# Optimization experiments

Measured on AMD Instinct MI355X. Metric: run time of the kernel, lower is better.

## Reference

```python
import jax, jax.numpy as jnp
import numpy as np

STRIDE = 16
NUM_A = 9
POS_TH, NEG_TH = 0.7, 0.3
FG, BG, IGN = 1.0, 0.0, 2.0
CAP = 128  # BATCH_SIZE * 0.5 for both fg and bg


def _generate_base_anchors(base_size=16, ratios=(0.5, 1.0, 2.0), scales=(8, 16, 32)):
    w = h = float(base_size)
    xc = yc = 0.5 * (base_size - 1)
    size = w * h
    out = []
    for r in ratios:
        ws = np.round(np.sqrt(size / r))
        hs = np.round(ws * r)
        for s in scales:
            W, H = ws * s, hs * s
            out.append([xc - 0.5 * (W - 1), yc - 0.5 * (H - 1),
                        xc + 0.5 * (W - 1), yc + 0.5 * (H - 1)])
    return np.asarray(out, dtype=np.float32)  # [9,4]


def _all_anchors(H, W):
    base = _generate_base_anchors()
    sx = np.arange(W, dtype=np.float32) * STRIDE
    sy = np.arange(H, dtype=np.float32) * STRIDE
    xs, ys = np.meshgrid(sx, sy)  # row-major over (h, w)
    shifts = np.stack([xs.ravel(), ys.ravel(), xs.ravel(), ys.ravel()], 1)
    return jnp.asarray((shifts[:, None, :] + base[None, :, :]).reshape(-1, 4))  # [H*W*9,4], order (h,w,a)


def _forward(scores, gt, im_w, im_h):
    H, W = scores.shape[2], scores.shape[3]
    anchors = _all_anchors(H, W)  # [N,4]
    valid = (anchors[:, 0] >= 0.) & (anchors[:, 1] >= 0.) & \
            (anchors[:, 2] < im_w) & (anchors[:, 3] < im_h)
    # pairwise IoU with +1 box convention
    aw = anchors[:, 2] - anchors[:, 0] + 1.
    ah = anchors[:, 3] - anchors[:, 1] + 1.
    a_area = jnp.where((aw > 0) & (ah > 0), aw * ah, 0.)
    gw = gt[:, 2] - gt[:, 0] + 1.
    gh = gt[:, 3] - gt[:, 1] + 1.
    g_area = jnp.where((gw > 0) & (gh > 0), gw * gh, 0.)
    ix1 = jnp.maximum(anchors[:, None, 0], gt[None, :, 0])
    iy1 = jnp.maximum(anchors[:, None, 1], gt[None, :, 1])
    ix2 = jnp.minimum(anchors[:, None, 2], gt[None, :, 2])
    iy2 = jnp.minimum(anchors[:, None, 3], gt[None, :, 3])
    iw = ix2 - ix1 + 1.
    ih = iy2 - iy1 + 1.
    inter = jnp.where((iw > 0) & (ih > 0), iw * ih, 0.)
    ovl = inter / (a_area[:, None] + g_area[None, :] - inter)  # [N,G]
    ovl_m = jnp.where(valid[:, None], ovl, -1.)  # exclude invalid anchors
    a_argmax = jnp.argmax(ovl, axis=1)           # best gt per anchor
    a_max = jnp.max(ovl, axis=1)
    g_max = jnp.max(ovl_m, axis=0)               # best (valid) anchor overlap per gt
    gt_fg = jnp.any(ovl_m == g_max[None, :], axis=1) & valid
    labels = jnp.where(valid & (a_max < NEG_TH), BG, IGN)
    labels = jnp.where(gt_fg, FG, labels)
    labels = jnp.where(valid & (a_max >= POS_TH), FG, labels)
    # random subsample fg/bg down to CAP each (matches npr.choice semantics in distribution)
    kf, kb = jax.random.split(jax.random.key(42))
    def subsample(lbl, mask, k):
        s = jnp.where(mask, jax.random.uniform(k, lbl.shape), jnp.inf)
        ranks = jnp.argsort(jnp.argsort(s))
        keep = ranks < jnp.minimum(jnp.sum(mask), CAP)
        return jnp.where(mask & ~keep, IGN, lbl)
    labels = subsample(labels, labels == FG, kf)
    labels = subsample(labels, labels == BG, kb)
    num_ni = jnp.sum(labels != IGN).astype(jnp.float32)
    gts = gt[a_argmax]
    ax = (anchors[:, 2] + anchors[:, 0]) * 0.5
    ay = (anchors[:, 3] + anchors[:, 1]) * 0.5
    gwm = gts[:, 2] - gts[:, 0] + 1.
    ghm = gts[:, 3] - gts[:, 1] + 1.
    gx = (gts[:, 2] + gts[:, 0]) * 0.5
    gy = (gts[:, 3] + gts[:, 1]) * 0.5
    adj = jnp.stack([(gx - ax) / aw, (gy - ay) / ah,
                     jnp.log(gwm / aw), jnp.log(ghm / ah)], axis=1)  # [N,4]
    adj = jnp.where(valid[:, None], adj, 0.)
    wts = jnp.where((labels == FG)[:, None], 1.0 / num_ni, 0.) * jnp.ones((1, 4), jnp.float32)
    labels_out = labels.reshape(1, H, W, NUM_A).transpose(0, 3, 1, 2) \
                       .reshape(1, 1, NUM_A * H, W).astype(jnp.int32)
    adj_out = adj.reshape(1, H, W, 4 * NUM_A).transpose(0, 3, 1, 2)
    wts_out = wts.reshape(1, H, W, 4 * NUM_A).transpose(0, 3, 1, 2)
    return labels_out, adj_out, wts_out


def setup_inputs() -> dict:
    key = jax.random.key(0)
    k1, k2, k3 = jax.random.split(key, 3)
    scores = jax.random.normal(k1, (1, 18, 256, 256), dtype=jnp.float32)
    G = 64
    cxy = jax.random.uniform(k2, (G, 2), minval=100., maxval=3900.)
    wh = jax.random.uniform(k3, (G, 2), minval=32., maxval=512.)
    x1y1 = jnp.clip(cxy - wh * 0.5, 0., 4095.)
    x2y2 = jnp.clip(cxy + wh * 0.5, 0., 4095.)
    gt = jnp.concatenate([x1y1, x2y2], axis=1)  # [G,4] = x1,y1,x2,y2
    return {"anchor_object_scores": scores, "ground_truth_boxes": gt,
            "im_w": 4096, "im_h": 4096}


def reference(anchor_object_scores, ground_truth_boxes, im_w, im_h):
    return _forward(anchor_object_scores, ground_truth_boxes, im_w, im_h)
```

## Files before the change

### kernel.cpp

```cpp
#include <hip/hip_runtime.h>
#include <stdint.h>


#define NUM_A 9
#define HW 65536
#define N_ANCH 589824
#define NG 64
#define CAPK 128u
#define NBIN 2048
#define BIN_SHIFT 12
#define CLIST_CAP 128u
#define NGRP 32
#define GATHER_CAP 2048u

#define LAB_BG 0u
#define LAB_FG 1u
#define LAB_IGN 2u

#define NBLK 576

#define OFF_HF    0
#define OFF_HB    NBIN
#define OFF_ROOTB (2*NBIN)
#define OFF_ROOTD (2*NBIN + 1)
#define OFF_SEL   4104
#define OFF_SUBB  4112
#define OFF_SUBD  (OFF_SUBB + 32*16)
#define OFF_CFLG  (OFF_SUBD + 32*16)
#define OFF_CCNTF (OFF_CFLG + 32*16)
#define OFF_CCNTB (OFF_CCNTF + 32*16)
#define CTRL_WORDS (OFF_CCNTB + 32*16)
#define OFF_CANDF CTRL_WORDS
#define OFF_CANDB (OFF_CANDF + 2*NGRP*CLIST_CAP)

#define MAGIC_C 0x5CA1AB1Eu

__constant__ float BA[NUM_A][4] = {
  { -84.f,  -40.f,  99.f,  55.f}, {-176.f,  -88.f, 191.f, 103.f},
  {-360.f, -184.f, 375.f, 199.f}, { -56.f,  -56.f,  71.f,  71.f},
  {-120.f, -120.f, 135.f, 135.f}, {-248.f, -248.f, 263.f, 263.f},
  { -36.f,  -80.f,  51.f,  95.f}, { -80.f, -168.f,  95.f, 183.f},
  {-168.f, -344.f, 183.f, 359.f}};

__host__ __device__ static inline void tf2x32(uint32_t k0, uint32_t k1,
                                              uint32_t x0, uint32_t x1,
                                              uint32_t* o0, uint32_t* o1) {
  const uint32_t ks2 = k0 ^ k1 ^ 0x1BD11BDAu;
#define TF_R(r) { x0 += x1; x1 = (x1 << (r)) | (x1 >> (32 - (r))); x1 ^= x0; }
  x0 += k0; x1 += k1;
  TF_R(13) TF_R(15) TF_R(26) TF_R(6)
  x0 += k1;  x1 += ks2 + 1u;
  TF_R(17) TF_R(29) TF_R(16) TF_R(24)
  x0 += ks2; x1 += k0 + 2u;
  TF_R(13) TF_R(15) TF_R(26) TF_R(6)
  x0 += k0;  x1 += k1 + 3u;
  TF_R(17) TF_R(29) TF_R(16) TF_R(24)
  x0 += k1;  x1 += ks2 + 4u;
  TF_R(13) TF_R(15) TF_R(26) TF_R(6)
  x0 += ks2; x1 += k0 + 5u;
#undef TF_R
  *o0 = x0; *o1 = x1;
}

__device__ static inline uint32_t mant_of(uint32_t k0, uint32_t k1, uint32_t n) {
  uint32_t o0, o1;
  tf2x32(k0, k1, 0u, n, &o0, &o1);
  return (o0 ^ o1) >> 9;
}

__device__ static inline float axis_best(float blo, float bhi, float glo,
                                         float ghi, int lo, int hi) {
  #pragma clang fp contract(off)
  float t1 = (ghi - bhi) * 0.0625f;
  float t2 = (glo - blo) * 0.0625f;
  float tmin = fminf(t1, t2), tmax = fmaxf(t1, t2);
  int c1 = (int)floorf(tmin), c2 = (int)ceilf(tmax);
  int cand0 = lo, cand1 = hi;
  int cand2 = min(max(c1,     lo), hi);
  int cand3 = min(max(c1 + 1, lo), hi);
  int cand4 = min(max(c2 - 1, lo), hi);
  int cand5 = min(max(c2,     lo), hi);
  float best = -3.0e38f;
  int cands[6] = {cand0, cand1, cand2, cand3, cand4, cand5};
  #pragma unroll
  for (int i = 0; i < 6; i++) {
    float s = (float)(cands[i] << 4);
    float v = fminf(bhi + s, ghi) - fmaxf(blo + s, glo) + 1.0f;
    best = fmaxf(best, v);
  }
  return best;
}

#define AG_LOAD(p)      __hip_atomic_load((p), __ATOMIC_RELAXED, __HIP_MEMORY_SCOPE_AGENT)
#define AG_STORE(p, v)  __hip_atomic_store((p), (v), __ATOMIC_RELAXED, __HIP_MEMORY_SCOPE_AGENT)

__global__ __launch_bounds__(256) void k_one(const float* __restrict__ gt,
                                             const int* __restrict__ imw_p,
                                             const int* __restrict__ imh_p,
                                             float* __restrict__ out_lab,
                                             float* __restrict__ out_adj,
                                             float* __restrict__ out_wts,
                                             uint32_t* __restrict__ ws,
                                             uint32_t kf0, uint32_t kf1,
                                             uint32_t kb0, uint32_t kb1) {
  #pragma clang fp contract(off)
  __shared__ uint64_t scB[GATHER_CAP];
  uint32_t* sh = (uint32_t*)scB;
  __shared__ float sg0[NG], sg1[NG], sg2[NG], sg3[NG], sga[NG], sgm[NG];
  __shared__ uint32_t sgmU[NG];
  __shared__ unsigned long long sMask[4];
  __shared__ int sAnyZero, sLastB, sLastD;
  __shared__ uint32_t sSel[8];
  __shared__ uint32_t sCnt[NGRP], sBase[NGRP], sTot;
  int tid = threadIdx.x;
  int b = blockIdx.x;
  int a = b >> 6, hb = (b & 63) << 2;

  {
    uint4* sh4 = (uint4*)sh;
    #pragma unroll
    for (int k = 0; k < 4; k++) sh4[tid + k * 256] = make_uint4(0, 0, 0, 0);
  }
  if (tid == 0) sAnyZero = 0;
  if (tid < NG) {
    const float4 g4 = ((const float4*)gt)[tid];
    sg0[tid] = g4.x; sg1[tid] = g4.y; sg2[tid] = g4.z; sg3[tid] = g4.w;
    float gw = g4.z - g4.x + 1.0f, gh = g4.w - g4.y + 1.0f;
    sga[tid] = (gw > 0.0f && gh > 0.0f) ? gw * gh : 0.0f;
    sgmU[tid] = 0u;
  }
  __syncthreads();

  {
    int imwi = imw_p[0], imhi = imh_p[0];
    for (int p = tid; p < NG * NUM_A; p += 256) {
      int g = p / NUM_A, q = p - g * NUM_A;
      float b0 = BA[q][0], b1 = BA[q][1], b2 = BA[q][2], b3 = BA[q][3];
      int ib0 = (int)b0, ib1 = (int)b1, ib2 = (int)b2, ib3 = (int)b3;
      int wlo = max(0, (-ib0 + 15) >> 4);
      int whi = min(255, (imwi - ib2 - 1) >> 4);
      int hlo = max(0, (-ib1 + 15) >> 4);
      int hhi = min(255, (imhi - ib3 - 1) >> 4);
      if (wlo > whi || hlo > hhi) continue;
      float iwb = axis_best(b0, b2, sg0[g], sg2[g], wlo, whi);
      float ihb = axis_best(b1, b3, sg1[g], sg3[g], hlo, hhi);
      float aw = b2 - b0 + 1.0f, ah = b3 - b1 + 1.0f;
      float aarea = aw * ah;
      float inter = (iwb > 0.0f && ihb > 0.0f) ? iwb * ihb : 0.0f;
      float den = aarea + sga[g] - inter;
      float o = inter / den;
      atomicMax(&sgmU[g], __float_as_uint(o));
    }
  }

  {
    int wv = tid >> 6, g = tid & 63;
    float sy = (float)((hb + wv) << 4);
    float ihp = fminf(BA[a][3] + sy, sg3[g]) - fmaxf(BA[a][1] + sy, sg1[g]) + 1.0f;
    unsigned long long mk = __ballot(ihp > 0.0f);
    if (g == 0) sMask[wv] = mk;
  }
  __syncthreads();
  if (tid < NG) {
    uint32_t mm = sgmU[tid];
    sgm[tid] = __uint_as_float(mm);
    if (mm == 0u) atomicOr(&sAnyZero, 1);
  }
  __syncthreads();

  float BA0 = BA[a][0], BA1 = BA[a][1], BA2 = BA[a][2], BA3 = BA[a][3];
  float imw = (float)imw_p[0], imh = (float)imh_p[0];
  int w = tid;
  float sx = (float)(w << 4);
  float A0 = BA0 + sx, A2 = BA2 + sx;
  float aw = A2 - A0 + 1.0f;
  float A1v[4], A3v[4];
  #pragma unroll
  for (int r = 0; r < 4; r++) {
    float sy = (float)((hb + r) << 4);
    A1v[r] = BA1 + sy; A3v[r] = BA3 + sy;
  }
  float ah = A3v[0] - A1v[0] + 1.0f;
  float aarea = aw * ah;
  bool xv = (A0 >= 0.0f) && (A2 < imw);

  unsigned long long mk0 = sMask[0], mk1 = sMask[1],
                     mk2 = sMask[2], mk3 = sMask[3];
  unsigned long long uni = mk0 | mk1 | mk2 | mk3;
  float amaxv[4] = {0.f, 0.f, 0.f, 0.f};
  int bgv[4] = {0, 0, 0, 0};
  uint32_t afv = 0u;
  while (uni) {
    int g = __ffsll(uni) - 1;
    uni &= uni - 1;
    float iw = fminf(A2, sg2[g]) - fmaxf(A0, sg0[g]) + 1.0f;
    if (!__any(iw > 0.0f)) continue;
    if (iw > 0.0f) {
      float base = aarea + sga[g];
      float gy1 = sg1[g], gy2 = sg3[g], gm = sgm[g];
#define DO_ROW(r, mk)                                                     \
      if ((mk >> g) & 1ull) {                                             \
        float ih = fminf(A3v[r], gy2) - fmaxf(A1v[r], gy1) + 1.0f;        \
        float inter = iw * ih;                                            \
        float o = inter / (base - inter);                                 \
        if (o > amaxv[r]) { amaxv[r] = o; bgv[r] = g; }                   \
        if (o == gm) afv |= (1u << r);                                    \
      }
      DO_ROW(0, mk0) DO_ROW(1, mk1) DO_ROW(2, mk2) DO_ROW(3, mk3)
#undef DO_ROW
    }
  }

  bool anyZ = (sAnyZero != 0);
  uint32_t lm[4];
  #pragma unroll
  for (int r = 0; r < 4; r++) {
    int hw = (hb + r) * 256 + w;
    bool valid = xv && (A1v[r] >= 0.0f) && (A3v[r] < imh);
    float amax = amaxv[r];
    bool anyfg = (((afv >> r) & 1u) || anyZ) && valid;
    uint32_t lab;
    if (!valid)                       lab = LAB_IGN;
    else if (anyfg || amax >= 0.7f)   lab = LAB_FG;
    else if (amax < 0.3f)             lab = LAB_BG;
    else                              lab = LAB_IGN;

    float adj0 = 0.f, adj1 = 0.f, adj2 = 0.f, adj3 = 0.f;
    if (valid) {
      int bg = bgv[r];
      float G0 = sg0[bg], G1 = sg1[bg], G2 = sg2[bg], G3 = sg3[bg];
      float ax = (A2 + A0) * 0.5f, ay = (A3v[r] + A1v[r]) * 0.5f;
      float gwm = G2 - G0 + 1.0f, ghm = G3 - G1 + 1.0f;
      float gx = (G2 + G0) * 0.5f, gy = (G3 + G1) * 0.5f;
      adj0 = (gx - ax) / aw;
      adj1 = (gy - ay) / ah;
      adj2 = logf(gwm / aw);
      adj3 = logf(ghm / ah);
    }
    int c4 = a * 4;
    out_adj[(c4 + 0) * HW + hw] = adj0;
    out_adj[(c4 + 1) * HW + hw] = adj1;
    out_adj[(c4 + 2) * HW + hw] = adj2;
    out_adj[(c4 + 3) * HW + hw] = adj3;

    uint32_t m = 0u;
    uint32_t n = (uint32_t)(hw * 9 + a);
    if (lab != LAB_IGN) {
      uint32_t kk0 = (lab == LAB_FG) ? kf0 : kb0;
      uint32_t kk1 = (lab == LAB_FG) ? kf1 : kb1;
      m = mant_of(kk0, kk1, n);
      atomicAdd(&sh[((lab == LAB_FG) ? 0 : NBIN) + (m >> BIN_SHIFT)], 1u);
    }
    lm[r] = (lab << 24) | m;
  }
  __syncthreads();

  for (int i = tid; i < 2 * NBIN; i += 256) {
    uint32_t v = sh[i];
    if (v) atomicAdd(&ws[OFF_HF + i], v);
  }
  asm volatile("s_waitcnt vmcnt(0)" ::: "memory");
  __syncthreads();

  if (tid == 0) {
    int last = 0;
    uint32_t v = atomicAdd(&ws[OFF_SUBB + (b & 31) * 16], 1u);
    if (v == 17u) {
      uint32_t r = atomicAdd(&ws[OFF_ROOTB], 1u);
      if (r == 31u) last = 1;
    }
    sLastB = last;
  }
  __syncthreads();
  if (sLastB) {
    for (int cls = 0; cls < 2; cls++) {
      uint32_t* hist = ws + (cls ? OFF_HB : OFF_HF);
      uint32_t* sel = ws + OFF_SEL + cls * 4;
      uint32_t loc[8], s = 0;
      #pragma unroll
      for (int j = 0; j < 8; j++) {
        loc[j] = AG_LOAD(&hist[tid * 8 + j]);
        s += loc[j];
      }
      sh[tid] = s; __syncthreads();
      for (int off = 1; off < 256; off <<= 1) {
        uint32_t v = (tid >= off) ? sh[tid - off] : 0u;
        __syncthreads();
        sh[tid] += v;
        __syncthreads();
      }
      uint32_t total = sh[255];
      uint32_t K = total < CAPK ? total : CAPK;
      if (tid == 0) {
        AG_STORE(&sel[3], K);
        if (K == 0u) {
          AG_STORE(&sel[0], 0xFFFFFFFFu); AG_STORE(&sel[1], 0u);
          AG_STORE(&sel[2], 0u);
        }
      }
      if (K > 0u) {
        uint32_t myC = sh[tid], pvC = (tid == 0) ? 0u : sh[tid - 1];
        if (myC >= K && pvC < K) {
          uint32_t cum = pvC; int bb = tid * 8;
          #pragma unroll
          for (int j = 0; j < 8; j++) {
            if (cum + loc[j] >= K) { bb = tid * 8 + j; break; }
            cum += loc[j];
          }
          AG_STORE(&sel[0], (uint32_t)bb); AG_STORE(&sel[1], cum);
          AG_STORE(&sel[2], K - cum);
        }
      }
      __syncthreads();
    }
    asm volatile("s_waitcnt vmcnt(0)" ::: "memory");
    __syncthreads();
    if (tid < 32) AG_STORE(&ws[OFF_CFLG + tid * 16], MAGIC_C);
  }

  if (tid == 0) {
    while (AG_LOAD(&ws[OFF_CFLG + (b & 31) * 16]) != MAGIC_C)
      __builtin_amdgcn_s_sleep(2);
  }
  __syncthreads();
  if (tid < 8) sSel[tid] = AG_LOAD(&ws[OFF_SEL + tid]);
  __syncthreads();
  uint32_t bf = sSel[0], Kf = sSel[3], bbn = sSel[4], Kb = sSel[7];
  float inv = 1.0f / (float)(Kf + Kb);

  uint32_t pushedMask = 0u;
  #pragma unroll
  for (int r = 0; r < 4; r++) {
    uint32_t lab = lm[r] >> 24;
    if (lab == LAB_IGN) continue;
    uint32_t m = lm[r] & 0x7FFFFFu;
    uint32_t bn = m >> BIN_SHIFT;
    uint32_t bnd = (lab == LAB_FG) ? bf : bbn;
    if (bn == bnd) {
      int hw = (hb + r) * 256 + w;
      uint32_t n = (uint32_t)(hw * 9 + a);
      uint32_t grp = (uint32_t)(b & 31);
      uint32_t cbase = (lab == LAB_FG) ? OFF_CCNTF : OFF_CCNTB;
      uint32_t idx = atomicAdd(&ws[cbase + grp * 16], 1u);
      if (idx < CLIST_CAP) {
        uint64_t* lst = (uint64_t*)(ws + ((lab == LAB_FG) ? OFF_CANDF
                                                          : OFF_CANDB)) +
                        grp * CLIST_CAP;
        AG_STORE(&lst[idx], ((uint64_t)m << 20) | (uint64_t)n);
        pushedMask |= (1u << r);
      }
    }
  }
  asm volatile("s_waitcnt vmcnt(0)" ::: "memory");
  __syncthreads();

  if (tid == 0) {
    int last = 0;
    uint32_t v = atomicAdd(&ws[OFF_SUBD + (b & 31) * 16], 1u);
    if (v == 17u) {
      uint32_t r = atomicAdd(&ws[OFF_ROOTD], 1u);
      if (r == 31u) last = 1;
    }
    sLastD = last;
  }
  __syncthreads();
  if (sLastD) {
    uint64_t* sc = scB;
    for (int cls = 0; cls < 2; cls++) {
      const uint64_t* lst0 =
          (const uint64_t*)(ws + (cls ? OFF_CANDB : OFF_CANDF));
      if (tid < NGRP) {
        uint32_t cg = AG_LOAD(&ws[(cls ? OFF_CCNTB : OFF_CCNTF) + tid * 16]);
        sCnt[tid] = cg < CLIST_CAP ? cg : CLIST_CAP;
      }
      __syncthreads();
      if (tid == 0) {
        uint32_t acc = 0;
        for (int g2 = 0; g2 < NGRP; g2++) { sBase[g2] = acc; acc += sCnt[g2]; }
        sTot = acc < GATHER_CAP ? acc : GATHER_CAP;
      }
      __syncthreads();
      for (uint32_t idx = tid; idx < NGRP * CLIST_CAP; idx += 256) {
        uint32_t grp = idx >> 7;
        uint32_t i = idx & (CLIST_CAP - 1u);
        if (i < sCnt[grp]) {
          uint32_t dst = sBase[grp] + i;
          if (dst < GATHER_CAP)
            sc[dst] = AG_LOAD(&lst0[grp * CLIST_CAP + i]);
        }
      }
      __syncthreads();
      uint32_t C = sTot;
      uint32_t need = AG_LOAD(&ws[OFF_SEL + cls * 4 + 2]);
      for (uint32_t i = tid; i < C; i += 256) {
        uint64_t k = sc[i];
        uint32_t rr = 0;
        for (uint32_t j = 0; j < C; j++) rr += (sc[j] < k) ? 1u : 0u;
        bool kept = (rr < need);
        uint32_t nn = (uint32_t)(k & 0xFFFFFu);
        uint32_t aa = nn % 9u, hww = nn / 9u;
        uint32_t tt = aa * HW + hww;
        float lv = kept ? (cls == 0 ? 1.0f : 0.0f) : 2.0f;
        float wvv = (kept && cls == 0) ? inv : 0.0f;
        AG_STORE(&out_lab[tt], lv);
        #pragma unroll
        for (int j2 = 0; j2 < 4; j2++)
          AG_STORE(&out_wts[(aa * 4 + j2) * HW + hww], wvv);
      }
      __syncthreads();
    }
  }

  #pragma unroll
  for (int r = 0; r < 4; r++) {
    if ((pushedMask >> r) & 1u) continue;
    int hw = (hb + r) * 256 + w;
    uint32_t lab = lm[r] >> 24;
    uint32_t m = lm[r] & 0x7FFFFFu;
    float outv = 2.0f, wv = 0.0f;
    if (lab == LAB_FG) {
      uint32_t bn = m >> BIN_SHIFT;
      if (bn < bf) { outv = 1.0f; wv = inv; }
    } else if (lab == LAB_BG) {
      uint32_t bn = m >> BIN_SHIFT;
      if (bn < bbn) outv = 0.0f;
    }
    out_lab[a * HW + hw] = outv;
    int c4 = a * 4;
    out_wts[(c4 + 0) * HW + hw] = wv;
    out_wts[(c4 + 1) * HW + hw] = wv;
    out_wts[(c4 + 2) * HW + hw] = wv;
    out_wts[(c4 + 3) * HW + hw] = wv;
  }
}

extern "C" void kernel_launch(void* const* d_in, const int* in_sizes, int n_in,
                              void* d_out, int out_size, void* d_ws,
                              size_t ws_size, hipStream_t stream) {
  const float* gt  = (const float*)d_in[1];
  const int*   imw = (const int*)d_in[2];
  const int*   imh = (const int*)d_in[3];
  float* out      = (float*)d_out;
  float* out_lab  = out;
  float* out_adj  = out + N_ANCH;
  float* out_wts  = out + 5 * N_ANCH;
  uint32_t* ws = (uint32_t*)d_ws;

  uint32_t kf0, kf1, kb0, kb1;
  tf2x32(0u, 42u, 0u, 0u, &kf0, &kf1);
  tf2x32(0u, 42u, 0u, 1u, &kb0, &kb1);

  hipMemsetAsync(ws, 0, CTRL_WORDS * sizeof(uint32_t), stream);
  hipLaunchKernelGGL(k_one, dim3(NBLK), dim3(256), 0, stream, gt, imw, imh,
                     out_lab, out_adj, out_wts, ws, kf0, kf1, kb0, kb1);
}
```

Baseline: 103.9 us.

## Replace histogram-based top-K selection with count-then-threshold sampling rounds

Drops the per-block shared-memory 2048-bin histograms and their global atomic merges for the fg and bg classes. Each block now only counts its fg and bg anchors. A single block derives a mantissa threshold aimed at about 512 candidates per class, and blocks push candidates below the threshold into hashed global lists. The last block of each round ranks those candidates to find the exact K-th key, or adjusts the threshold and triggers another round, up to 8 grid-wide rounds. This cuts atomic traffic, but each extra round adds another grid-wide spin barrier, and the result depends on every block being resident at once.

```diff
diff --git a/kernel.cpp b/kernel.cpp
--- a/kernel.cpp
+++ b/kernel.cpp
@@ -7,11 +7,6 @@
 #define N_ANCH 589824
 #define NG 64
 #define CAPK 128u
-#define NBIN 2048
-#define BIN_SHIFT 12
-#define CLIST_CAP 128u
-#define NGRP 32
-#define GATHER_CAP 2048u
 
 #define LAB_BG 0u
 #define LAB_FG 1u
@@ -19,19 +14,31 @@
 
 #define NBLK 576
 
-#define OFF_HF    0
-#define OFF_HB    NBIN
-#define OFF_ROOTB (2*NBIN)
-#define OFF_ROOTD (2*NBIN + 1)
-#define OFF_SEL   4104
-#define OFF_SUBB  4112
-#define OFF_SUBD  (OFF_SUBB + 32*16)
-#define OFF_CFLG  (OFF_SUBD + 32*16)
-#define OFF_CCNTF (OFF_CFLG + 32*16)
-#define OFF_CCNTB (OFF_CCNTF + 32*16)
-#define CTRL_WORDS (OFF_CCNTB + 32*16)
-#define OFF_CANDF CTRL_WORDS
-#define OFF_CANDB (OFF_CANDF + 2*NGRP*CLIST_CAP)
+#define NGRP 32
+#define GCAP 256u
+#define R_MAX 8
+#define TARGETC 512u
+#define TFULL (1u << 23)
+#define CLIMIT 1024u
+#define GATHER_CAP 2048u
+
+#define OFF_CNTF  0
+#define OFF_CNTB  512
+#define OFF_SUBB  1024
+#define OFF_ROOTB 1536
+#define OFF_SELB  1552
+#define OFF_CFLGB 1568
+#define OFF_RND   2080
+#define RSTRIDE   2080
+#define R_SUBD    0
+#define R_ROOTD   512
+#define R_DCMD    528
+#define R_CFLGD   544
+#define R_PCNTF   1056
+#define R_PCNTB   1568
+#define CTRL_WORDS (OFF_RND + R_MAX * RSTRIDE)
+#define OFF_LISTF CTRL_WORDS
+#define OFF_LISTB (OFF_LISTF + 2 * NGRP * GCAP)
 
 #define MAGIC_C 0x5CA1AB1Eu
 
@@ -105,23 +112,18 @@
                                              uint32_t kb0, uint32_t kb1) {
   #pragma clang fp contract(off)
   __shared__ uint64_t scB[GATHER_CAP];
-  uint32_t* sh = (uint32_t*)scB;
   __shared__ float sg0[NG], sg1[NG], sg2[NG], sg3[NG], sga[NG], sgm[NG];
   __shared__ uint32_t sgmU[NG];
   __shared__ unsigned long long sMask[4];
-  __shared__ int sAnyZero, sLastB, sLastD;
-  __shared__ uint32_t sSel[8];
-  __shared__ uint32_t sCnt[NGRP], sBase[NGRP], sTot;
+  __shared__ int sAnyZero, sLastB, sLastD, sOv;
+  __shared__ uint32_t sSel[12];
+  __shared__ uint32_t sCnt[NGRP], sBase[NGRP], sTot, sBkLo, sBkHi;
+  __shared__ uint32_t sCF, sCB;
   int tid = threadIdx.x;
   int b = blockIdx.x;
   int a = b >> 6, hb = (b & 63) << 2;
 
-  {
-    uint4* sh4 = (uint4*)sh;
-    #pragma unroll
-    for (int k = 0; k < 4; k++) sh4[tid + k * 256] = make_uint4(0, 0, 0, 0);
-  }
-  if (tid == 0) sAnyZero = 0;
+  if (tid == 0) { sAnyZero = 0; sCF = 0u; sCB = 0u; }
   if (tid < NG) {
     const float4 g4 = ((const float4*)gt)[tid];
     sg0[tid] = g4.x; sg1[tid] = g4.y; sg2[tid] = g4.z; sg3[tid] = g4.w;
@@ -213,6 +215,7 @@
 
   bool anyZ = (sAnyZero != 0);
   uint32_t lm[4];
+  uint32_t cfLoc = 0, cbLoc = 0;
   #pragma unroll
   for (int r = 0; r < 4; r++) {
     int hw = (hb + r) * 256 + w;
@@ -249,181 +252,209 @@
       uint32_t kk0 = (lab == LAB_FG) ? kf0 : kb0;
       uint32_t kk1 = (lab == LAB_FG) ? kf1 : kb1;
       m = mant_of(kk0, kk1, n);
-      atomicAdd(&sh[((lab == LAB_FG) ? 0 : NBIN) + (m >> BIN_SHIFT)], 1u);
+      if (lab == LAB_FG) cfLoc++; else cbLoc++;
     }
     lm[r] = (lab << 24) | m;
   }
-  __syncthreads();
-
-  for (int i = tid; i < 2 * NBIN; i += 256) {
-    uint32_t v = sh[i];
-    if (v) atomicAdd(&ws[OFF_HF + i], v);
-  }
-  asm volatile("s_waitcnt vmcnt(0)" ::: "memory");
+  if (cfLoc) atomicAdd(&sCF, cfLoc);
+  if (cbLoc) atomicAdd(&sCB, cbLoc);
   __syncthreads();
 
   if (tid == 0) {
+    if (sCF) atomicAdd(&ws[OFF_CNTF + (b & 31) * 16], sCF);
+    if (sCB) atomicAdd(&ws[OFF_CNTB + (b & 31) * 16], sCB);
+    asm volatile("s_waitcnt vmcnt(0)" ::: "memory");
     int last = 0;
     uint32_t v = atomicAdd(&ws[OFF_SUBB + (b & 31) * 16], 1u);
     if (v == 17u) {
-      uint32_t r = atomicAdd(&ws[OFF_ROOTB], 1u);
-      if (r == 31u) last = 1;
+      uint32_t q = atomicAdd(&ws[OFF_ROOTB], 1u);
+      if (q == 31u) last = 1;
     }
     sLastB = last;
   }
   __syncthreads();
   if (sLastB) {
-    for (int cls = 0; cls < 2; cls++) {
-      uint32_t* hist = ws + (cls ? OFF_HB : OFF_HF);
-      uint32_t* sel = ws + OFF_SEL + cls * 4;
-      uint32_t loc[8], s = 0;
-      #pragma unroll
-      for (int j = 0; j < 8; j++) {
-        loc[j] = AG_LOAD(&hist[tid * 8 + j]);
-        s += loc[j];
-      }
-      sh[tid] = s; __syncthreads();
-      for (int off = 1; off < 256; off <<= 1) {
-        uint32_t v = (tid >= off) ? sh[tid - off] : 0u;
+    if (tid < 32)       sCnt[tid] = AG_LOAD(&ws[OFF_CNTF + tid * 16]);
+    else if (tid < 64)  sBase[tid - 32] = AG_LOAD(&ws[OFF_CNTB + (tid - 32) * 16]);
+    __syncthreads();
+    if (tid == 0) {
+      uint32_t tf = 0, tb = 0;
+      for (int i = 0; i < 32; i++) { tf += sCnt[i]; tb += sBase[i]; }
+      uint32_t Kf_ = tf < CAPK ? tf : CAPK;
+      uint32_t Kb_ = tb < CAPK ? tb : CAPK;
+      uint32_t Tf_ = (tf <= TARGETC) ? TFULL
+                   : (uint32_t)(((unsigned long long)TARGETC << 23) / tf);
+      uint32_t Tb_ = (tb <= TARGETC) ? TFULL
+                   : (uint32_t)(((unsigned long long)TARGETC << 23) / tb);
+      if (Tf_ == 0u) Tf_ = 1u;
+      if (Tb_ == 0u) Tb_ = 1u;
+      AG_STORE(&ws[OFF_SELB + 0], Tf_); AG_STORE(&ws[OFF_SELB + 1], Tb_);
+      AG_STORE(&ws[OFF_SELB + 2], Kf_); AG_STORE(&ws[OFF_SELB + 3], Kb_);
+      AG_STORE(&ws[OFF_SELB + 4], tf);  AG_STORE(&ws[OFF_SELB + 5], tb);
+    }
+    asm volatile("s_waitcnt vmcnt(0)" ::: "memory");
+    __syncthreads();
+    if (tid < 32) AG_STORE(&ws[OFF_CFLGB + tid * 16], MAGIC_C);
+  }
+
+  if (tid == 0) {
+    while (AG_LOAD(&ws[OFF_CFLGB + (b & 31) * 16]) != MAGIC_C)
+      __builtin_amdgcn_s_sleep(2);
+  }
+  __syncthreads();
+  if (tid < 6) sSel[tid] = AG_LOAD(&ws[OFF_SELB + tid]);
+  __syncthreads();
+  uint32_t Tc[2] = {sSel[0], sSel[1]};
+  uint32_t Kf = sSel[2], Kb = sSel[3], totF = sSel[4], totB = sSel[5];
+  float inv = 1.0f / (float)(Kf + Kb);
+
+  uint32_t modeF = 0u, modeB = 0u;
+  uint64_t bkF = 0ull, bkB = 0ull;
+  bool doneSel = false;
+  for (int rnd = 0; rnd < R_MAX && !doneSel; rnd++) {
+    uint32_t base = OFF_RND + (uint32_t)rnd * RSTRIDE;
+    #pragma unroll
+    for (int r = 0; r < 4; r++) {
+      uint32_t lab = lm[r] >> 24;
+      if (lab == LAB_IGN) continue;
+      uint32_t m = lm[r] & 0x7FFFFFu;
+      int cls = (lab == LAB_FG) ? 0 : 1;
+      if (m < Tc[cls]) {
+        int hw = (hb + r) * 256 + w;
+        uint32_t n = (uint32_t)(hw * 9 + a);
+        uint32_t grp = (n * 2654435761u) >> 27;
+        uint32_t idx = atomicAdd(
+            &ws[base + (cls ? R_PCNTB : R_PCNTF) + grp * 16], 1u);
+        if (idx < GCAP) {
+          uint64_t* lst =
+              (uint64_t*)(ws + (cls ? OFF_LISTB : OFF_LISTF)) + grp * GCAP;
+          AG_STORE(&lst[idx], ((uint64_t)m << 20) | (uint64_t)n);
+        }
+      }
+    }
+    asm volatile("s_waitcnt vmcnt(0)" ::: "memory");
+    __syncthreads();
+    if (tid == 0) {
+      int last = 0;
+      uint32_t v = atomicAdd(&ws[base + R_SUBD + (b & 31) * 16], 1u);
+      if (v == 17u) {
+        uint32_t q = atomicAdd(&ws[base + R_ROOTD], 1u);
+        if (q == 31u) last = 1;
+      }
+      sLastD = last;
+    }
+    __syncthreads();
+    if (sLastD) {
+      uint32_t modes[2]; uint64_t bks[2]; int oks[2];
+      uint32_t Cs[2]; int ovs[2];
+      for (int cls = 0; cls < 2; cls++) {
+        uint32_t Kc = cls ? Kb : Kf;
+        uint32_t totc = cls ? totB : totF;
+        if (tid < 32)
+          sCnt[tid] = AG_LOAD(&ws[base + (cls ? R_PCNTB : R_PCNTF) + tid * 16]);
         __syncthreads();
-        sh[tid] += v;
+        if (tid == 0) {
+          uint32_t acc = 0; int ov = 0;
+          for (int g2 = 0; g2 < NGRP; g2++) {
+            uint32_t c2 = sCnt[g2];
+            if (c2 > GCAP) { ov = 1; c2 = GCAP; }
+            sBase[g2] = acc; acc += c2;
+          }
+          sTot = acc; sOv = ov;
+        }
         __syncthreads();
-      }
-      uint32_t total = sh[255];
-      uint32_t K = total < CAPK ? total : CAPK;
+        uint32_t C = sTot; int ov = sOv;
+        uint32_t mode = 0u; uint64_t bk = 0ull; int ok = 1;
+        if (Kc == 0u) { ok = 1; mode = 0u; }
+        else if (totc <= CAPK) { ok = (!ov && C == totc); mode = 1u; }
+        else {
+          ok = (!ov && C >= Kc && C <= CLIMIT &&
+                (totc > TARGETC || C == totc));
+          mode = 2u;
+        }
+        if (ok && mode == 2u) {
+          const uint64_t* lst0 =
+              (const uint64_t*)(ws + (cls ? OFF_LISTB : OFF_LISTF));
+          for (uint32_t idx = tid; idx < NGRP * GCAP; idx += 256) {
+            uint32_t g2 = idx >> 8, i = idx & 255u;
+            if (i < sCnt[g2]) {
+              uint32_t dst = sBase[g2] + i;
+              if (dst < GATHER_CAP)
+                scB[dst] = AG_LOAD(&lst0[g2 * GCAP + i]);
+            }
+          }
+          __syncthreads();
+          for (uint32_t i = tid; i < C; i += 256) {
+            uint64_t k = scB[i];
+            uint32_t rr = 0;
+            for (uint32_t j = 0; j < C; j++) rr += (scB[j] < k) ? 1u : 0u;
+            if (rr == Kc - 1u) {
+              sBkLo = (uint32_t)k; sBkHi = (uint32_t)(k >> 32);
+            }
+          }
+          __syncthreads();
+          bk = ((uint64_t)sBkHi << 32) | (uint64_t)sBkLo;
+        }
+        modes[cls] = mode; bks[cls] = bk; oks[cls] = ok;
+        Cs[cls] = C; ovs[cls] = ov;
+        __syncthreads();
+      }
+      uint32_t st = (oks[0] && oks[1]) ? 1u : 2u;
+      uint32_t TN[2];
+      for (int cls = 0; cls < 2; cls++) {
+        uint32_t t = Tc[cls];
+        if (!oks[cls]) {
+          if (ovs[cls] || Cs[cls] > CLIMIT) t = (t > 1u) ? (t >> 1) : 1u;
+          else { t = (t >= (TFULL >> 2)) ? TFULL : (t << 2); }
+        }
+        TN[cls] = t;
+      }
       if (tid == 0) {
-        AG_STORE(&sel[3], K);
-        if (K == 0u) {
-          AG_STORE(&sel[0], 0xFFFFFFFFu); AG_STORE(&sel[1], 0u);
-          AG_STORE(&sel[2], 0u);
-        }
-      }
-      if (K > 0u) {
-        uint32_t myC = sh[tid], pvC = (tid == 0) ? 0u : sh[tid - 1];
-        if (myC >= K && pvC < K) {
-          uint32_t cum = pvC; int bb = tid * 8;
-          #pragma unroll
-          for (int j = 0; j < 8; j++) {
-            if (cum + loc[j] >= K) { bb = tid * 8 + j; break; }
-            cum += loc[j];
-          }
-          AG_STORE(&sel[0], (uint32_t)bb); AG_STORE(&sel[1], cum);
-          AG_STORE(&sel[2], K - cum);
-        }
-      }
+        AG_STORE(&ws[base + R_DCMD + 0], st);
+        AG_STORE(&ws[base + R_DCMD + 1], modes[0]);
+        AG_STORE(&ws[base + R_DCMD + 2], (uint32_t)bks[0]);
+        AG_STORE(&ws[base + R_DCMD + 3], (uint32_t)(bks[0] >> 32));
+        AG_STORE(&ws[base + R_DCMD + 4], modes[1]);
+        AG_STORE(&ws[base + R_DCMD + 5], (uint32_t)bks[1]);
+        AG_STORE(&ws[base + R_DCMD + 6], (uint32_t)(bks[1] >> 32));
+        AG_STORE(&ws[base + R_DCMD + 7], TN[0]);
+        AG_STORE(&ws[base + R_DCMD + 8], TN[1]);
+      }
+      asm volatile("s_waitcnt vmcnt(0)" ::: "memory");
       __syncthreads();
-    }
-    asm volatile("s_waitcnt vmcnt(0)" ::: "memory");
-    __syncthreads();
-    if (tid < 32) AG_STORE(&ws[OFF_CFLG + tid * 16], MAGIC_C);
-  }
-
-  if (tid == 0) {
-    while (AG_LOAD(&ws[OFF_CFLG + (b & 31) * 16]) != MAGIC_C)
-      __builtin_amdgcn_s_sleep(2);
-  }
-  __syncthreads();
-  if (tid < 8) sSel[tid] = AG_LOAD(&ws[OFF_SEL + tid]);
-  __syncthreads();
-  uint32_t bf = sSel[0], Kf = sSel[3], bbn = sSel[4], Kb = sSel[7];
-  float inv = 1.0f / (float)(Kf + Kb);
-
-  uint32_t pushedMask = 0u;
+      if (tid < 32) AG_STORE(&ws[base + R_CFLGD + tid * 16], MAGIC_C);
+    }
+    if (tid == 0) {
+      while (AG_LOAD(&ws[base + R_CFLGD + (b & 31) * 16]) != MAGIC_C)
+        __builtin_amdgcn_s_sleep(2);
+    }
+    __syncthreads();
+    if (tid < 9) sSel[tid] = AG_LOAD(&ws[base + R_DCMD + tid]);
+    __syncthreads();
+    if (sSel[0] == 1u) {
+      modeF = sSel[1]; bkF = ((uint64_t)sSel[3] << 32) | (uint64_t)sSel[2];
+      modeB = sSel[4]; bkB = ((uint64_t)sSel[6] << 32) | (uint64_t)sSel[5];
+      doneSel = true;
+    } else {
+      Tc[0] = sSel[7]; Tc[1] = sSel[8];
+    }
+    __syncthreads();
+  }
+
   #pragma unroll
   for (int r = 0; r < 4; r++) {
-    uint32_t lab = lm[r] >> 24;
-    if (lab == LAB_IGN) continue;
-    uint32_t m = lm[r] & 0x7FFFFFu;
-    uint32_t bn = m >> BIN_SHIFT;
-    uint32_t bnd = (lab == LAB_FG) ? bf : bbn;
-    if (bn == bnd) {
-      int hw = (hb + r) * 256 + w;
-      uint32_t n = (uint32_t)(hw * 9 + a);
-      uint32_t grp = (uint32_t)(b & 31);
-      uint32_t cbase = (lab == LAB_FG) ? OFF_CCNTF : OFF_CCNTB;
-      uint32_t idx = atomicAdd(&ws[cbase + grp * 16], 1u);
-      if (idx < CLIST_CAP) {
-        uint64_t* lst = (uint64_t*)(ws + ((lab == LAB_FG) ? OFF_CANDF
-                                                          : OFF_CANDB)) +
-                        grp * CLIST_CAP;
-        AG_STORE(&lst[idx], ((uint64_t)m << 20) | (uint64_t)n);
-        pushedMask |= (1u << r);
-      }
-    }
-  }
-  asm volatile("s_waitcnt vmcnt(0)" ::: "memory");
-  __syncthreads();
-
-  if (tid == 0) {
-    int last = 0;
-    uint32_t v = atomicAdd(&ws[OFF_SUBD + (b & 31) * 16], 1u);
-    if (v == 17u) {
-      uint32_t r = atomicAdd(&ws[OFF_ROOTD], 1u);
-      if (r == 31u) last = 1;
-    }
-    sLastD = last;
-  }
-  __syncthreads();
-  if (sLastD) {
-    uint64_t* sc = scB;
-    for (int cls = 0; cls < 2; cls++) {
-      const uint64_t* lst0 =
-          (const uint64_t*)(ws + (cls ? OFF_CANDB : OFF_CANDF));
-      if (tid < NGRP) {
-        uint32_t cg = AG_LOAD(&ws[(cls ? OFF_CCNTB : OFF_CCNTF) + tid * 16]);
-        sCnt[tid] = cg < CLIST_CAP ? cg : CLIST_CAP;
-      }
-      __syncthreads();
-      if (tid == 0) {
-        uint32_t acc = 0;
-        for (int g2 = 0; g2 < NGRP; g2++) { sBase[g2] = acc; acc += sCnt[g2]; }
-        sTot = acc < GATHER_CAP ? acc : GATHER_CAP;
-      }
-      __syncthreads();
-      for (uint32_t idx = tid; idx < NGRP * CLIST_CAP; idx += 256) {
-        uint32_t grp = idx >> 7;
-        uint32_t i = idx & (CLIST_CAP - 1u);
-        if (i < sCnt[grp]) {
-          uint32_t dst = sBase[grp] + i;
-          if (dst < GATHER_CAP)
-            sc[dst] = AG_LOAD(&lst0[grp * CLIST_CAP + i]);
-        }
-      }
-      __syncthreads();
-      uint32_t C = sTot;
-      uint32_t need = AG_LOAD(&ws[OFF_SEL + cls * 4 + 2]);
-      for (uint32_t i = tid; i < C; i += 256) {
-        uint64_t k = sc[i];
-        uint32_t rr = 0;
-        for (uint32_t j = 0; j < C; j++) rr += (sc[j] < k) ? 1u : 0u;
-        bool kept = (rr < need);
-        uint32_t nn = (uint32_t)(k & 0xFFFFFu);
-        uint32_t aa = nn % 9u, hww = nn / 9u;
-        uint32_t tt = aa * HW + hww;
-        float lv = kept ? (cls == 0 ? 1.0f : 0.0f) : 2.0f;
-        float wvv = (kept && cls == 0) ? inv : 0.0f;
-        AG_STORE(&out_lab[tt], lv);
-        #pragma unroll
-        for (int j2 = 0; j2 < 4; j2++)
-          AG_STORE(&out_wts[(aa * 4 + j2) * HW + hww], wvv);
-      }
-      __syncthreads();
-    }
-  }
-
-  #pragma unroll
-  for (int r = 0; r < 4; r++) {
-    if ((pushedMask >> r) & 1u) continue;
     int hw = (hb + r) * 256 + w;
     uint32_t lab = lm[r] >> 24;
     uint32_t m = lm[r] & 0x7FFFFFu;
+    uint32_t n = (uint32_t)(hw * 9 + a);
+    uint64_t key = ((uint64_t)m << 20) | (uint64_t)n;
     float outv = 2.0f, wv = 0.0f;
     if (lab == LAB_FG) {
-      uint32_t bn = m >> BIN_SHIFT;
-      if (bn < bf) { outv = 1.0f; wv = inv; }
+      bool kept = (modeF == 1u) || (modeF == 2u && key <= bkF);
+      if (kept) { outv = 1.0f; wv = inv; }
     } else if (lab == LAB_BG) {
-      uint32_t bn = m >> BIN_SHIFT;
-      if (bn < bbn) outv = 0.0f;
+      bool kept = (modeB == 1u) || (modeB == 2u && key <= bkB);
+      if (kept) outv = 0.0f;
     }
     out_lab[a * HW + hw] = outv;
     int c4 = a * 4;
```

After: 227.5 us. +118.9%, slower.
